# Kernel tuning notes

Hardware: AMD Instinct MI355X
Metric: run time of the kernel (lower is better)

## Reference

```python
import jax, jax.numpy as jnp
import numpy as np

NEG_INF = -jnp.inf  # aggregation identity for the max-plus semifield


def setup_inputs() -> dict:
    key = jax.random.key(0)
    k1, k2, k3 = jax.random.split(key, 3)
    B, C_in, C_out, H, W, M, N = 4, 32, 32, 80, 80, 5, 5
    x = jax.random.normal(k1, (B, C_in, H, W), dtype=jnp.float32)
    w = jax.random.normal(k2, (C_out, C_in, M, N), dtype=jnp.float32) * 0.1
    bias = jax.random.normal(k3, (C_out,), dtype=jnp.float32) * 0.1
    return {"x": x, "w": w, "bias": bias}


def reference(x, w, bias):
    """Max-plus semifield conv: out[b,co,h,w] = bias[co] + sum_ci max_{m,n} (x_pad[b,ci,h+m,w+n] + w[co,ci,m,n]).

    Faithful to SemiConv2d._semi_conv with semifield = (amax, add, -inf, 0),
    but computed with a running max over the MN taps instead of materializing
    the [B, C_out, C_in, M*N, H*W] tensor the torch code builds via unfold.
    """
    B, C_in, H, W = x.shape
    C_out, _, M, N = w.shape
    # padding exactly as in _semi_conv (odd vs even kernel), fill = aggregation identity
    pt, pb = (M // 2, M // 2) if M % 2 else (M // 2 - 1, M // 2)
    pl, pr = (N // 2, N // 2) if N % 2 else (N // 2 - 1, N // 2)
    xp = jnp.pad(x, ((0, 0), (0, 0), (pt, pb), (pl, pr)), constant_values=NEG_INF)
    # running max over the M*N taps (fixed small loop, not a data-dim loop)
    acc = jnp.full((B, C_out, C_in, H, W), NEG_INF, dtype=x.dtype)
    for m in range(M):
        for n in range(N):
            patch = xp[:, :, m:m + H, n:n + W]               # [B, C_in, H, W]
            tap = patch[:, None] + w[None, :, :, m, n, None, None]  # [B, C_out, C_in, H, W]
            acc = jnp.maximum(acc, tap)
    out = jnp.sum(acc, axis=2) + bias[None, :, None, None]   # sum over C_in, add bias
    return out
```

## Files before the change

### kernel.cpp

```cpp
#include <hip/hip_runtime.h>
#include <math.h>

#define CIN  32
#define COUT 32
#define BB   4
#define HH   80
#define WW   80
#define HW   (HH * WW)
#define NOUT (BB * COUT * HW)
#define TH   16
#define XR   20
#define XC   88
#define TILE (XR * XC)
#define WSLICE 352
#define NT   320

typedef float v4f __attribute__((ext_vector_type(4)));

__device__ __forceinline__ float max3f(float a, float b, float c) {
    float d;
    asm("v_max3_f32 %0, %1, %2, %3" : "=v"(d) : "v"(a), "v"(b), "v"(c));
    return d;
}

__device__ __forceinline__ void load_lds4(const float* g, float* l) {
    __builtin_amdgcn_global_load_lds(
        (const __attribute__((address_space(1))) void*)g,
        (__attribute__((address_space(3))) void*)l, 4, 0, 0);
}

template<int NP>
__global__ __launch_bounds__(NT, 7) void semiconv_kernel(
    const float* __restrict__ x,
    const float* __restrict__ w,
    const float* __restrict__ bias,
    float* __restrict__ dst)
{
    constexpr int CP = CIN / NP;
    __shared__ __align__(16) float xs[3][TILE];
    __shared__ __align__(16) float wl[CP * 60];
    __shared__ __align__(16) float trash[64];

    const int tid = threadIdx.x;
    const int bh  = blockIdx.x;
    const int cp  = blockIdx.y;
    const int zz  = blockIdx.z;
    const int b    = zz / NP;
    const int part = zz % NP;
    const int ci0  = part * CP;
    const int h0   = bh * TH;
    const int co0  = cp * 2;

    const int lane = tid & 63;
    const int wave = tid >> 6;
    const int wslot = wave * WSLICE;

    for (int idx = tid; idx < CP * 50; idx += NT) {
        int run = idx / (CP * 25);
        int r   = idx % (CP * 25);
        int k = r / 25, t = r % 25, m = t / 5, n = t % 5;
        wl[k * 60 + m * 12 + n * 2 + run] =
            w[((size_t)(co0 + run) * CIN + ci0) * 25 + r];
    }
    __builtin_amdgcn_sched_barrier(0);

    int goff[6];
    #pragma unroll
    for (int j = 0; j < 6; ++j) {
        int idx = wslot + j * 64 + lane;
        bool valid = (j < 5) || (lane < 32);
        int r = idx / XC, c = idx % XC;
        int gr = h0 + r - 2, gc = c - 2;
        bool in = valid && gr >= 0 && gr < HH && gc >= 0 && gc < WW;
        goff[j] = in ? (gr * WW + gc) : -1;
        if (valid && !in) {
            xs[0][idx] = -INFINITY; xs[1][idx] = -INFINITY; xs[2][idx] = -INFINITY;
        }
    }

    const float* xbase = x + (size_t)(b * CIN + ci0) * HW;

    auto issue_tile = [&](int t, int bf) {
        const float* xp = xbase + (size_t)t * HW;
        #pragma unroll
        for (int j = 0; j < 6; ++j) {
            bool pred = (goff[j] >= 0);
            if (__any(pred)) {
                if (pred) load_lds4(xp + goff[j], &xs[bf][wslot + j * 64]);
            } else {
                load_lds4(xp, &trash[0]);
            }
        }
    };

    issue_tile(0, 0);
    issue_tile(1, 1);

    const int ty = tid / 20, tx = tid % 20, wc = tx * 4;
    const int xro = ty * XC + wc;
    float sA[4] = {0.f, 0.f, 0.f, 0.f}, sB[4] = {0.f, 0.f, 0.f, 0.f};

    asm volatile("s_waitcnt vmcnt(6) lgkmcnt(0)" ::: "memory");
    __builtin_amdgcn_s_barrier();
    __builtin_amdgcn_sched_barrier(0);

    #pragma unroll
    for (int k = 0; k < CP; ++k) {
        if (k + 2 < CP) issue_tile(k + 2, (k + 2) % 3);

        const float* xk = &xs[k % 3][xro];
        const float* wk = wl + k * 60;
        float aA[4], aB[4];
        #pragma unroll
        for (int m = 0; m < 5; ++m) {
            v4f A  = *(const v4f*)(xk + m * XC);
            v4f C  = *(const v4f*)(xk + m * XC + 4);
            v4f W0 = *(const v4f*)(wk + m * 12);
            v4f W1 = *(const v4f*)(wk + m * 12 + 4);
            v4f W2 = *(const v4f*)(wk + m * 12 + 8);
            float xr[8] = {A.x, A.y, A.z, A.w, C.x, C.y, C.z, C.w};
            float wa[5] = {W0.x, W0.z, W1.x, W1.z, W2.x};
            float wb[5] = {W0.y, W0.w, W1.y, W1.w, W2.y};
            #pragma unroll
            for (int j = 0; j < 4; ++j) {
                float t = max3f(xr[j] + wa[0], xr[j+1] + wa[1], xr[j+2] + wa[2]);
                float u = fmaxf(xr[j+3] + wa[3], xr[j+4] + wa[4]);
                aA[j] = (m == 0) ? fmaxf(t, u) : max3f(aA[j], t, u);
                t = max3f(xr[j] + wb[0], xr[j+1] + wb[1], xr[j+2] + wb[2]);
                u = fmaxf(xr[j+3] + wb[3], xr[j+4] + wb[4]);
                aB[j] = (m == 0) ? fmaxf(t, u) : max3f(aB[j], t, u);
            }
        }
        #pragma unroll
        for (int j = 0; j < 4; ++j) { sA[j] += aA[j]; sB[j] += aB[j]; }

        if (k < CP - 2) {
            asm volatile("s_waitcnt vmcnt(6) lgkmcnt(0)" ::: "memory");
        } else if (k == CP - 2) {
            asm volatile("s_waitcnt vmcnt(0) lgkmcnt(0)" ::: "memory");
        }
        if (k < CP - 1) {
            __builtin_amdgcn_s_barrier();
            __builtin_amdgcn_sched_barrier(0);
        }
    }

    size_t oiA = (((size_t)b * COUT + co0) * HH + (h0 + ty)) * WW + wc;
    size_t oiB = oiA + (size_t)HW;
    v4f rA = {sA[0], sA[1], sA[2], sA[3]};
    v4f rB = {sB[0], sB[1], sB[2], sB[3]};
    float* o = dst;
    if (NP == 1) {
        float bcA = bias[co0], bcB = bias[co0 + 1];
        rA.x += bcA; rA.y += bcA; rA.z += bcA; rA.w += bcA;
        rB.x += bcB; rB.y += bcB; rB.z += bcB; rB.w += bcB;
    } else {
        o += (size_t)part * NOUT;
    }
    *(v4f*)(o + oiA) = rA;
    *(v4f*)(o + oiB) = rB;
}

template<int NP>
__global__ __launch_bounds__(256) void reduceN_kernel(
    const float* __restrict__ ws, const float* __restrict__ bias,
    float* __restrict__ out)
{
    int i4 = blockIdx.x * 256 + threadIdx.x;
    const float4* p = reinterpret_cast<const float4*>(ws);
    float4 r = p[i4];
    #pragma unroll
    for (int q = 1; q < NP; ++q) {
        float4 t = p[i4 + (size_t)q * (NOUT / 4)];
        r.x += t.x; r.y += t.y; r.z += t.z; r.w += t.w;
    }
    int co = (i4 / (HW / 4)) & (COUT - 1);
    float bc = bias[co];
    r.x += bc; r.y += bc; r.z += bc; r.w += bc;
    reinterpret_cast<float4*>(out)[i4] = r;
}

__global__ __launch_bounds__(256) void naive_kernel(
    const float* __restrict__ x, const float* __restrict__ w,
    const float* __restrict__ bias, float* __restrict__ out)
{
    int o = blockIdx.x * 256 + threadIdx.x;
    if (o >= NOUT) return;
    int wcol = o % WW, h = (o / WW) % HH, co = (o / HW) % COUT, b = o / (COUT * HW);
    float sum = 0.f;
    for (int ci = 0; ci < CIN; ++ci) {
        float mx = -INFINITY;
        for (int m = 0; m < 5; ++m) {
            int gr = h + m - 2;
            if (gr < 0 || gr >= HH) continue;
            for (int n = 0; n < 5; ++n) {
                int gc = wcol + n - 2;
                if (gc < 0 || gc >= WW) continue;
                float v = x[((size_t)(b * CIN + ci)) * HW + gr * WW + gc]
                        + w[((size_t)(co * CIN + ci)) * 25 + m * 5 + n];
                mx = fmaxf(mx, v);
            }
        }
        sum += mx;
    }
    out[o] = sum + bias[co];
}

extern "C" void kernel_launch(void* const* d_in, const int* in_sizes, int n_in,
                              void* d_out, int out_size, void* d_ws, size_t ws_size,
                              hipStream_t stream) {
    const float* x    = (const float*)d_in[0];
    const float* w    = (const float*)d_in[1];
    const float* bias = (const float*)d_in[2];
    float* out        = (float*)d_out;

    const size_t need4 = 4ull * NOUT * sizeof(float);
    const size_t need2 = 2ull * NOUT * sizeof(float);

    if (ws_size >= need4) {
        dim3 grid(HH / TH, COUT / 2, BB * 4);
        semiconv_kernel<4><<<grid, NT, 0, stream>>>(x, w, bias, (float*)d_ws);
        reduceN_kernel<4><<<NOUT / 4 / 256, 256, 0, stream>>>((const float*)d_ws, bias, out);
    } else if (ws_size >= need2) {
        dim3 grid(HH / TH, COUT / 2, BB * 2);
        semiconv_kernel<2><<<grid, NT, 0, stream>>>(x, w, bias, (float*)d_ws);
        reduceN_kernel<2><<<NOUT / 4 / 256, 256, 0, stream>>>((const float*)d_ws, bias, out);
    } else {
        naive_kernel<<<(NOUT + 255) / 256, 256, 0, stream>>>(x, w, bias, out);
    }
}
```

Measured before the change: 40.70 us.

## Pre-pad input into workspace and read directly from global memory, drop LDS staging

Adds a pad kernel that writes a -inf padded copy of x (row stride 88) and a 28-stride padded weight array into the workspace. The conv kernel then reads x rows and weights straight from global memory through the cache, instead of triple-buffering tiles in LDS with async global-to-LDS loads and barriers. This removes LDS traffic, barriers and boundary handling from the main kernel. In exchange it adds an extra launch plus a full write and reread of the padded input, and relies on cache hits for the overlapping window reads. The mid-size workspace fallback now runs the unsplit NP=1 variant instead of NP=2.

Result: no change. 41.32 us (+1.5%).

```diff
diff --git a/kernel.cpp b/kernel.cpp
--- a/kernel.cpp
+++ b/kernel.cpp
@@ -9,11 +9,15 @@
 #define HW   (HH * WW)
 #define NOUT (BB * COUT * HW)
 #define TH   16
-#define XR   20
-#define XC   88
-#define TILE (XR * XC)
-#define WSLICE 352
 #define NT   320
+
+#define XPS  88
+#define XPR  84
+#define XPLANE (XPR * XPS)
+#define XPAD_SZ (BB * CIN * XPLANE)
+#define WPAD_OFF 1048576
+#define WPAD_SZ (COUT * CIN * 28)
+#define PART_OFF 2097152
 
 typedef float v4f __attribute__((ext_vector_type(4)));
 
@@ -23,24 +27,36 @@
     return d;
 }
 
-__device__ __forceinline__ void load_lds4(const float* g, float* l) {
-    __builtin_amdgcn_global_load_lds(
-        (const __attribute__((address_space(1))) void*)g,
-        (__attribute__((address_space(3))) void*)l, 4, 0, 0);
+__global__ __launch_bounds__(256) void pad_kernel(
+    const float* __restrict__ x, const float* __restrict__ w,
+    float* __restrict__ ws)
+{
+    int idx = blockIdx.x * 256 + threadIdx.x;
+    int stride = gridDim.x * 256;
+    for (int i = idx; i < XPAD_SZ; i += stride) {
+        int c = i % XPS;
+        int t = i / XPS;
+        int r = t % XPR;
+        int p = t / XPR;
+        int gr = r - 2, gc = c - 2;
+        float v = -INFINITY;
+        if (gr >= 0 && gr < HH && gc >= 0 && gc < WW)
+            v = x[(size_t)p * HW + gr * WW + gc];
+        ws[i] = v;
+    }
+    for (int i = idx; i < WPAD_SZ; i += stride) {
+        int q = i % 28, p = i / 28;
+        ws[WPAD_OFF + i] = (q < 28 && q < 25) ? w[p * 25 + q] : 0.0f;
+    }
 }
 
 template<int NP>
 __global__ __launch_bounds__(NT, 7) void semiconv_kernel(
-    const float* __restrict__ x,
-    const float* __restrict__ w,
+    const float* __restrict__ ws,
     const float* __restrict__ bias,
     float* __restrict__ dst)
 {
     constexpr int CP = CIN / NP;
-    __shared__ __align__(16) float xs[3][TILE];
-    __shared__ __align__(16) float wl[CP * 60];
-    __shared__ __align__(16) float trash[64];
-
     const int tid = threadIdx.x;
     const int bh  = blockIdx.x;
     const int cp  = blockIdx.y;
@@ -48,104 +64,61 @@
     const int b    = zz / NP;
     const int part = zz % NP;
     const int ci0  = part * CP;
-    const int h0   = bh * TH;
     const int co0  = cp * 2;
 
-    const int lane = tid & 63;
-    const int wave = tid >> 6;
-    const int wslot = wave * WSLICE;
-
-    for (int idx = tid; idx < CP * 50; idx += NT) {
-        int run = idx / (CP * 25);
-        int r   = idx % (CP * 25);
-        int k = r / 25, t = r % 25, m = t / 5, n = t % 5;
-        wl[k * 60 + m * 12 + n * 2 + run] =
-            w[((size_t)(co0 + run) * CIN + ci0) * 25 + r];
-    }
-    __builtin_amdgcn_sched_barrier(0);
-
-    int goff[6];
-    #pragma unroll
-    for (int j = 0; j < 6; ++j) {
-        int idx = wslot + j * 64 + lane;
-        bool valid = (j < 5) || (lane < 32);
-        int r = idx / XC, c = idx % XC;
-        int gr = h0 + r - 2, gc = c - 2;
-        bool in = valid && gr >= 0 && gr < HH && gc >= 0 && gc < WW;
-        goff[j] = in ? (gr * WW + gc) : -1;
-        if (valid && !in) {
-            xs[0][idx] = -INFINITY; xs[1][idx] = -INFINITY; xs[2][idx] = -INFINITY;
+    const int ty = tid / 20, tx = tid % 20;
+    const int row = bh * TH + ty;
+    const int j0  = 4 * tx;
+
+    const float* xp = ws + ((size_t)(b * CIN + ci0) * XPR + row) * XPS + j0;
+    const float* wpA = ws + WPAD_OFF + ((size_t)(co0    ) * CIN + ci0) * 28;
+    const float* wpB = ws + WPAD_OFF + ((size_t)(co0 + 1) * CIN + ci0) * 28;
+
+    float sA[4] = {0.f, 0.f, 0.f, 0.f}, sB[4] = {0.f, 0.f, 0.f, 0.f};
+
+    #pragma unroll 1
+    for (int k = 0; k < CP; ++k) {
+        float wA[25], wB[25];
+        #pragma unroll
+        for (int q = 0; q < 25; ++q) { wA[q] = wpA[q]; wB[q] = wpB[q]; }
+
+        float xr[5][8];
+        #pragma unroll
+        for (int m = 0; m < 5; ++m) {
+            v4f A = *(const v4f*)(xp + m * XPS);
+            v4f C = *(const v4f*)(xp + m * XPS + 4);
+            xr[m][0] = A.x; xr[m][1] = A.y; xr[m][2] = A.z; xr[m][3] = A.w;
+            xr[m][4] = C.x; xr[m][5] = C.y; xr[m][6] = C.z; xr[m][7] = C.w;
         }
-    }
-
-    const float* xbase = x + (size_t)(b * CIN + ci0) * HW;
-
-    auto issue_tile = [&](int t, int bf) {
-        const float* xp = xbase + (size_t)t * HW;
-        #pragma unroll
-        for (int j = 0; j < 6; ++j) {
-            bool pred = (goff[j] >= 0);
-            if (__any(pred)) {
-                if (pred) load_lds4(xp + goff[j], &xs[bf][wslot + j * 64]);
-            } else {
-                load_lds4(xp, &trash[0]);
-            }
-        }
-    };
-
-    issue_tile(0, 0);
-    issue_tile(1, 1);
-
-    const int ty = tid / 20, tx = tid % 20, wc = tx * 4;
-    const int xro = ty * XC + wc;
-    float sA[4] = {0.f, 0.f, 0.f, 0.f}, sB[4] = {0.f, 0.f, 0.f, 0.f};
-
-    asm volatile("s_waitcnt vmcnt(6) lgkmcnt(0)" ::: "memory");
-    __builtin_amdgcn_s_barrier();
-    __builtin_amdgcn_sched_barrier(0);
-
-    #pragma unroll
-    for (int k = 0; k < CP; ++k) {
-        if (k + 2 < CP) issue_tile(k + 2, (k + 2) % 3);
-
-        const float* xk = &xs[k % 3][xro];
-        const float* wk = wl + k * 60;
+
         float aA[4], aB[4];
         #pragma unroll
         for (int m = 0; m < 5; ++m) {
-            v4f A  = *(const v4f*)(xk + m * XC);
-            v4f C  = *(const v4f*)(xk + m * XC + 4);
-            v4f W0 = *(const v4f*)(wk + m * 12);
-            v4f W1 = *(const v4f*)(wk + m * 12 + 4);
-            v4f W2 = *(const v4f*)(wk + m * 12 + 8);
-            float xr[8] = {A.x, A.y, A.z, A.w, C.x, C.y, C.z, C.w};
-            float wa[5] = {W0.x, W0.z, W1.x, W1.z, W2.x};
-            float wb[5] = {W0.y, W0.w, W1.y, W1.w, W2.y};
             #pragma unroll
             for (int j = 0; j < 4; ++j) {
-                float t = max3f(xr[j] + wa[0], xr[j+1] + wa[1], xr[j+2] + wa[2]);
-                float u = fmaxf(xr[j+3] + wa[3], xr[j+4] + wa[4]);
+                float t = max3f(xr[m][j]     + wA[5*m],
+                                xr[m][j + 1] + wA[5*m + 1],
+                                xr[m][j + 2] + wA[5*m + 2]);
+                float u = fmaxf(xr[m][j + 3] + wA[5*m + 3],
+                                xr[m][j + 4] + wA[5*m + 4]);
                 aA[j] = (m == 0) ? fmaxf(t, u) : max3f(aA[j], t, u);
-                t = max3f(xr[j] + wb[0], xr[j+1] + wb[1], xr[j+2] + wb[2]);
-                u = fmaxf(xr[j+3] + wb[3], xr[j+4] + wb[4]);
+                t = max3f(xr[m][j]     + wB[5*m],
+                          xr[m][j + 1] + wB[5*m + 1],
+                          xr[m][j + 2] + wB[5*m + 2]);
+                u = fmaxf(xr[m][j + 3] + wB[5*m + 3],
+                          xr[m][j + 4] + wB[5*m + 4]);
                 aB[j] = (m == 0) ? fmaxf(t, u) : max3f(aB[j], t, u);
             }
         }
         #pragma unroll
         for (int j = 0; j < 4; ++j) { sA[j] += aA[j]; sB[j] += aB[j]; }
 
-        if (k < CP - 2) {
-            asm volatile("s_waitcnt vmcnt(6) lgkmcnt(0)" ::: "memory");
-        } else if (k == CP - 2) {
-            asm volatile("s_waitcnt vmcnt(0) lgkmcnt(0)" ::: "memory");
-        }
-        if (k < CP - 1) {
-            __builtin_amdgcn_s_barrier();
-            __builtin_amdgcn_sched_barrier(0);
-        }
-    }
-
-    size_t oiA = (((size_t)b * COUT + co0) * HH + (h0 + ty)) * WW + wc;
+        xp  += XPLANE;
+        wpA += 28;
+        wpB += 28;
+    }
+
+    size_t oiA = (((size_t)b * COUT + co0) * HH + row) * WW + j0;
     size_t oiB = oiA + (size_t)HW;
     v4f rA = {sA[0], sA[1], sA[2], sA[3]};
     v4f rB = {sB[0], sB[1], sB[2], sB[3]};
@@ -163,11 +136,11 @@
 
 template<int NP>
 __global__ __launch_bounds__(256) void reduceN_kernel(
-    const float* __restrict__ ws, const float* __restrict__ bias,
+    const float* __restrict__ part, const float* __restrict__ bias,
     float* __restrict__ out)
 {
     int i4 = blockIdx.x * 256 + threadIdx.x;
-    const float4* p = reinterpret_cast<const float4*>(ws);
+    const float4* p = reinterpret_cast<const float4*>(part);
     float4 r = p[i4];
     #pragma unroll
     for (int q = 1; q < NP; ++q) {
@@ -213,18 +186,20 @@
     const float* w    = (const float*)d_in[1];
     const float* bias = (const float*)d_in[2];
     float* out        = (float*)d_out;
-
-    const size_t need4 = 4ull * NOUT * sizeof(float);
-    const size_t need2 = 2ull * NOUT * sizeof(float);
+    float* ws         = (float*)d_ws;
+
+    const size_t need4 = (size_t)(PART_OFF + 4ull * NOUT) * sizeof(float);
+    const size_t need1 = (size_t)PART_OFF * sizeof(float);
 
     if (ws_size >= need4) {
+        pad_kernel<<<1024, 256, 0, stream>>>(x, w, ws);
         dim3 grid(HH / TH, COUT / 2, BB * 4);
-        semiconv_kernel<4><<<grid, NT, 0, stream>>>(x, w, bias, (float*)d_ws);
-        reduceN_kernel<4><<<NOUT / 4 / 256, 256, 0, stream>>>((const float*)d_ws, bias, out);
-    } else if (ws_size >= need2) {
-        dim3 grid(HH / TH, COUT / 2, BB * 2);
-        semiconv_kernel<2><<<grid, NT, 0, stream>>>(x, w, bias, (float*)d_ws);
-        reduceN_kernel<2><<<NOUT / 4 / 256, 256, 0, stream>>>((const float*)d_ws, bias, out);
+        semiconv_kernel<4><<<grid, NT, 0, stream>>>(ws, bias, ws + PART_OFF);
+        reduceN_kernel<4><<<NOUT / 4 / 256, 256, 0, stream>>>(ws + PART_OFF, bias, out);
+    } else if (ws_size >= need1) {
+        pad_kernel<<<1024, 256, 0, stream>>>(x, w, ws);
+        dim3 grid(HH / TH, COUT / 2, BB);
+        semiconv_kernel<1><<<grid, NT, 0, stream>>>(ws, bias, out);
     } else {
         naive_kernel<<<(NOUT + 255) / 256, 256, 0, stream>>>(x, w, bias, out);
     }
```
